# Kernel tuning notes

Hardware: AMD Instinct MI355X
Metric: run time of the kernel (lower is better)

The kernel has to match this reference:

```python
import jax, jax.numpy as jnp
import numpy as np

EMBED_DIM = 1024
NUM_HEADS = 8
HEAD_DIM = EMBED_DIM // NUM_HEADS
SCALING = HEAD_DIM ** -0.5
SEQ_LEN = 2048
BATCH = 4


def setup_inputs() -> dict:
    key = jax.random.key(0)
    ks = jax.random.split(key, 12)
    s = 0.02
    d = EMBED_DIM
    return {
        "q": jax.random.normal(ks[0], (SEQ_LEN, BATCH, d), jnp.float32),
        "k": jax.random.normal(ks[1], (SEQ_LEN, BATCH, d), jnp.float32),
        "v": jax.random.normal(ks[2], (SEQ_LEN, BATCH, d), jnp.float32),
        # Linear weights stored as (in, out): y = x @ W + b
        "Wq": jax.random.normal(ks[3], (d, d), jnp.float32) * s,
        "bq": jnp.zeros((d,), jnp.float32),
        "Wk": jax.random.normal(ks[4], (d, d), jnp.float32) * s,
        "bk": jnp.zeros((d,), jnp.float32),
        "Wv": jax.random.normal(ks[5], (d, d), jnp.float32) * s,
        "bv": jnp.zeros((d,), jnp.float32),
        "Wo": jax.random.normal(ks[6], (d, d), jnp.float32) * s,
        "bo": jnp.zeros((d,), jnp.float32),
    }


def _to_head(x):
    # 'l n (h e) -> n h l e'
    l, n, _ = x.shape
    return x.reshape(l, n, NUM_HEADS, HEAD_DIM).transpose(1, 2, 0, 3)


def reference(q, k, v, Wq, bq, Wk, bk, Wv, bv, Wo, bo):
    l = q.shape[0]  # src_len
    m = k.shape[0]  # tgt_len
    qp = (q @ Wq + bq) * SCALING          # (l, n, d)
    kp = k @ Wk + bk                       # (m, n, d)
    vp = v @ Wv + bv                       # (m, n, d) -- V shared across heads
    qh = _to_head(qp)                      # (n, h, l, e)
    kh = _to_head(kp)                      # (n, h, m, e)
    scores = jnp.einsum('nhle,nhme->nhlm', qh, kh)  # (n, h, l, m)
    mask = jnp.triu(jnp.ones((l, m), bool), k=1)    # True above diagonal
    scores = jnp.where(mask[None, None], -jnp.inf, scores)
    w = jax.nn.softmax(scores, axis=-1)    # (n, h, l, m)
    w_mean = w.mean(axis=1)                # head-averaged weights (n, l, m)
    attn = jnp.einsum('nlm,mne->lne', w_mean, vp)   # (l, n, d)
    out = attn @ Wo + bo                   # (l, n, d)
    return out, w_mean
```

## Files before the change

### kernel.cpp

```cpp
#include <hip/hip_runtime.h>


#define L_SEQ 2048
#define NBATCH 4
#define DMODEL 1024
#define NHEAD 8
#define SCALING 0.08838834764831845f
#define NQ (2048L * 4 * 1024)

typedef _Float16 f16x8 __attribute__((ext_vector_type(8)));
typedef float f32x4 __attribute__((ext_vector_type(4)));

#define GLOBAL_AS __attribute__((address_space(1)))
#define LDS_AS __attribute__((address_space(3)))

__device__ __forceinline__ unsigned short f2h_bits(float x) {
  _Float16 h = (_Float16)x;
  return __builtin_bit_cast(unsigned short, h);
}

__device__ __forceinline__ void gl_lds16(const void* g, void* l) {
  __builtin_amdgcn_global_load_lds((GLOBAL_AS void*)g, (LDS_AS void*)l, 16, 0, 0);
}

__global__ __launch_bounds__(256) void zero1(float4* __restrict__ a, long n4)
{
  float4 z = {0.f, 0.f, 0.f, 0.f};
  long stride = (long)gridDim.x * 256;
  for (long i = (long)blockIdx.x * 256 + threadIdx.x; i < n4; i += stride)
    a[i] = z;
}

__global__ __launch_bounds__(256) void cvt3(
    const float* __restrict__ q, const float* __restrict__ k,
    const float* __restrict__ v, _Float16* __restrict__ xh)
{
  long i = ((long)blockIdx.x * 256 + threadIdx.x) * 8;
  if (i >= 3 * NQ) return;
  int which = (int)(i / NQ);
  const float* src = which == 0 ? q : (which == 1 ? k : v);
  long off = i - (long)which * NQ;
  float4 a = *(const float4*)(src + off);
  float4 b = *(const float4*)(src + off + 4);
  f16x8 h;
  h[0] = (_Float16)a.x; h[1] = (_Float16)a.y; h[2] = (_Float16)a.z; h[3] = (_Float16)a.w;
  h[4] = (_Float16)b.x; h[5] = (_Float16)b.y; h[6] = (_Float16)b.z; h[7] = (_Float16)b.w;
  *(f16x8*)(xh + i) = h;
}

template <bool AF16, bool BF16>
__global__ __launch_bounds__(256) void gemm16(
    const void* __restrict__ Ap, long lda, long a_bs,
    const void* __restrict__ Bp, long ldb, long b_bs,
    float* __restrict__ C, long ldc, long c_bs,
    _Float16* __restrict__ Ch, long ldch, long ch_bs,
    const float* __restrict__ bias, int bias_row, float alpha, int K,
    int causal, int cmode)
{
  __shared__ __align__(16) _Float16 As[128][64];
  __shared__ __align__(16) _Float16 Bs[128][64];
  const int tid = threadIdx.x;
  const int lane = tid & 63, wv = tid >> 6;
  const int g = lane >> 4, cc = lane & 15;
  const int wm = wv >> 1, wn = wv & 1;
  const long m0 = (long)blockIdx.y * 128;
  const long n0 = (long)blockIdx.x * 128;

  const float* Af = nullptr; const _Float16* Ah = nullptr;
  const float* Bf = nullptr; const _Float16* Bh = nullptr;
  if constexpr (AF16) Ah = (const _Float16*)Ap + (long)blockIdx.z * a_bs;
  else                Af = (const float*)Ap + (long)blockIdx.z * a_bs;
  if constexpr (BF16) Bh = (const _Float16*)Bp + (long)blockIdx.z * b_bs;
  else                Bf = (const float*)Bp + (long)blockIdx.z * b_bs;

  int Keff = K;
  if (causal) { int lim = (int)m0 + 128; if (lim < K) Keff = lim; }
  const int NT = Keff >> 6;

  f32x4 acc[4][4] = {};
  char* AsB = (char*)&As[0][0];
  char* BsB = (char*)&Bs[0][0];

  for (int kt = 0; kt < NT; ++kt) {
    const long k0 = (long)kt << 6;
    __syncthreads();
    if constexpr (AF16) {
#pragma unroll
      for (int i = 0; i < 4; ++i) {
        int r = 32 * wv + 8 * i + (lane >> 3);
        int gc = (lane & 7) ^ (r & 7);
        gl_lds16(Ah + (m0 + r) * lda + k0 + gc * 8, &As[32 * wv + 8 * i][0]);
      }
    } else {
#pragma unroll
      for (int p = 0; p < 8; ++p) {
        int r = p * 16 + (tid >> 4);
        float4 vv = *(const float4*)(Af + (m0 + r) * lda + k0 + (tid & 15) * 4);
        ushort4 hh;
        hh.x = f2h_bits(vv.x); hh.y = f2h_bits(vv.y);
        hh.z = f2h_bits(vv.z); hh.w = f2h_bits(vv.w);
        *(ushort4*)(AsB + r * 128 + (((tid & 15) * 8) ^ ((r & 7) << 4))) = hh;
      }
    }
    if constexpr (BF16) {
#pragma unroll
      for (int i = 0; i < 4; ++i) {
        int r = 32 * wv + 8 * i + (lane >> 3);
        int gc = (lane & 7) ^ (r & 7);
        gl_lds16(Bh + (n0 + r) * ldb + k0 + gc * 8, &Bs[32 * wv + 8 * i][0]);
      }
    } else {
#pragma unroll
      for (int p = 0; p < 8; ++p) {
        int r = p * 16 + (tid >> 4);
        float4 vv = *(const float4*)(Bf + (n0 + r) * ldb + k0 + (tid & 15) * 4);
        ushort4 hh;
        hh.x = f2h_bits(vv.x); hh.y = f2h_bits(vv.y);
        hh.z = f2h_bits(vv.z); hh.w = f2h_bits(vv.w);
        *(ushort4*)(BsB + r * 128 + (((tid & 15) * 8) ^ ((r & 7) << 4))) = hh;
      }
    }
    __syncthreads();
#pragma unroll
    for (int s = 0; s < 2; ++s) {
      f16x8 af[4], bfr[4];
#pragma unroll
      for (int mi = 0; mi < 4; ++mi) {
        int r = wm * 64 + mi * 16 + cc;
        af[mi] = *(const f16x8*)(AsB + r * 128 + ((s * 64 + 16 * g) ^ ((r & 7) << 4)));
      }
#pragma unroll
      for (int ni = 0; ni < 4; ++ni) {
        int r = wn * 64 + ni * 16 + cc;
        bfr[ni] = *(const f16x8*)(BsB + r * 128 + ((s * 64 + 16 * g) ^ ((r & 7) << 4)));
      }
#pragma unroll
      for (int mi = 0; mi < 4; ++mi)
#pragma unroll
        for (int ni = 0; ni < 4; ++ni)
          acc[mi][ni] = __builtin_amdgcn_mfma_f32_16x16x32_f16(af[mi], bfr[ni], acc[mi][ni], 0, 0, 0);
    }
  }

  float* Cp = C ? C + (long)blockIdx.z * c_bs : nullptr;
  _Float16* Chp = Ch ? Ch + (long)blockIdx.z * ch_bs : nullptr;
#pragma unroll
  for (int ni = 0; ni < 4; ++ni) {
    long col = n0 + wn * 64 + ni * 16 + cc;
    float bcol = (bias && !bias_row) ? bias[col] : 0.0f;
#pragma unroll
    for (int mi = 0; mi < 4; ++mi) {
      long row0 = m0 + wm * 64 + mi * 16 + 4 * g;
#pragma unroll
      for (int rg = 0; rg < 4; ++rg) {
        long row = row0 + rg;
        float b = (bias && bias_row) ? bias[row] : bcol;
        float vv = (acc[mi][ni][rg] + b) * alpha;
        if (Cp) Cp[row * ldc + col] = vv;
        if (Chp) {
          if (cmode == 1) {
            long idx = (((row & 3) * NHEAD + (col >> 7)) * (long)L_SEQ + (row >> 2)) * 128 +
                       (col & 127);
            Chp[idx] = (_Float16)vv;
          } else {
            Chp[row * ldch + col] = (_Float16)vv;
          }
        }
      }
    }
  }
}

__global__ __launch_bounds__(256) void projqk(
    const _Float16* __restrict__ xh, const _Float16* __restrict__ WqT,
    const _Float16* __restrict__ WkT, const float* __restrict__ bq,
    const float* __restrict__ bk, _Float16* __restrict__ qph,
    _Float16* __restrict__ kph)
{
  __shared__ __align__(16) _Float16 As[64][64];
  __shared__ __align__(16) _Float16 Bs[128][64];
  const int tid = threadIdx.x, lane = tid & 63, wv = tid >> 6;
  const int g = lane >> 4, cc = lane & 15;
  const int wm = wv >> 1, wn = wv & 1;
  const int sel = (int)blockIdx.y;
  const _Float16* A = xh + (long)sel * NQ;
  const _Float16* B = sel ? WkT : WqT;
  const float* bias = sel ? bk : bq;
  const float alpha = sel ? 1.0f : SCALING;
  _Float16* dst = sel ? kph : qph;
  const int fi = (int)blockIdx.x;
  const long m0 = (long)(fi >> 3) * 64;
  const long n0 = (long)(fi & 7) * 128;

  f32x4 acc[2][4] = {};
  char* AsB = (char*)&As[0][0];
  char* BsB = (char*)&Bs[0][0];

  for (int kt = 0; kt < 16; ++kt) {
    const long k0 = (long)kt << 6;
    __syncthreads();
#pragma unroll
    for (int i = 0; i < 2; ++i) {
      int r = 16 * wv + 8 * i + (lane >> 3);
      int gc = (lane & 7) ^ (r & 7);
      gl_lds16(A + (m0 + r) * 1024 + k0 + gc * 8, &As[16 * wv + 8 * i][0]);
    }
#pragma unroll
    for (int i = 0; i < 4; ++i) {
      int r = 32 * wv + 8 * i + (lane >> 3);
      int gc = (lane & 7) ^ (r & 7);
      gl_lds16(B + (n0 + r) * 1024 + k0 + gc * 8, &Bs[32 * wv + 8 * i][0]);
    }
    __syncthreads();
#pragma unroll
    for (int s = 0; s < 2; ++s) {
      f16x8 af[2], bfr[4];
#pragma unroll
      for (int mi = 0; mi < 2; ++mi) {
        int r = wm * 32 + mi * 16 + cc;
        af[mi] = *(const f16x8*)(AsB + r * 128 + ((s * 64 + 16 * g) ^ ((r & 7) << 4)));
      }
#pragma unroll
      for (int ni = 0; ni < 4; ++ni) {
        int r = wn * 64 + ni * 16 + cc;
        bfr[ni] = *(const f16x8*)(BsB + r * 128 + ((s * 64 + 16 * g) ^ ((r & 7) << 4)));
      }
#pragma unroll
      for (int mi = 0; mi < 2; ++mi)
#pragma unroll
        for (int ni = 0; ni < 4; ++ni)
          acc[mi][ni] = __builtin_amdgcn_mfma_f32_16x16x32_f16(af[mi], bfr[ni], acc[mi][ni], 0, 0, 0);
    }
  }

#pragma unroll
  for (int ni = 0; ni < 4; ++ni) {
    long col = n0 + wn * 64 + ni * 16 + cc;
    float bcol = bias[col];
#pragma unroll
    for (int mi = 0; mi < 2; ++mi) {
      long row0 = m0 + wm * 32 + mi * 16 + 4 * g;
#pragma unroll
      for (int rg = 0; rg < 4; ++rg) {
        long row = row0 + rg;
        float vv = (acc[mi][ni][rg] + bcol) * alpha;
        long idx = (((row & 3) * NHEAD + (col >> 7)) * (long)L_SEQ + (row >> 2)) * 128 +
                   (col & 127);
        dst[idx] = (_Float16)vv;
      }
    }
  }
}

__global__ __launch_bounds__(256) void proj64(
    const _Float16* __restrict__ Ap, long lda, long a_bs,
    const _Float16* __restrict__ Bp, long ldb, long b_bs,
    _Float16* __restrict__ Ch, long ldch, long ch_bs,
    const float* __restrict__ bias, int bias_row, float alpha, int K,
    int cmode, int ntiles)
{
  __shared__ __align__(16) _Float16 As[64][64];
  __shared__ __align__(16) _Float16 Bs[128][64];
  const int tid = threadIdx.x, lane = tid & 63, wv = tid >> 6;
  const int g = lane >> 4, cc = lane & 15;
  const int wm = wv >> 1, wn = wv & 1;
  const int fi = (int)blockIdx.x;
  const int by = fi / ntiles, nc = fi % ntiles;
  const long m0 = (long)by * 64;
  const long n0 = (long)nc * 128;
  const _Float16* A = Ap + (long)blockIdx.z * a_bs;
  const _Float16* B = Bp + (long)blockIdx.z * b_bs;
  const int NT = K >> 6;

  f32x4 acc[2][4] = {};
  char* AsB = (char*)&As[0][0];
  char* BsB = (char*)&Bs[0][0];

  for (int kt = 0; kt < NT; ++kt) {
    const long k0 = (long)kt << 6;
    __syncthreads();
#pragma unroll
    for (int i = 0; i < 2; ++i) {
      int r = 16 * wv + 8 * i + (lane >> 3);
      int gc = (lane & 7) ^ (r & 7);
      gl_lds16(A + (m0 + r) * lda + k0 + gc * 8, &As[16 * wv + 8 * i][0]);
    }
#pragma unroll
    for (int i = 0; i < 4; ++i) {
      int r = 32 * wv + 8 * i + (lane >> 3);
      int gc = (lane & 7) ^ (r & 7);
      gl_lds16(B + (n0 + r) * ldb + k0 + gc * 8, &Bs[32 * wv + 8 * i][0]);
    }
    __syncthreads();
#pragma unroll
    for (int s = 0; s < 2; ++s) {
      f16x8 af[2], bfr[4];
#pragma unroll
      for (int mi = 0; mi < 2; ++mi) {
        int r = wm * 32 + mi * 16 + cc;
        af[mi] = *(const f16x8*)(AsB + r * 128 + ((s * 64 + 16 * g) ^ ((r & 7) << 4)));
      }
#pragma unroll
      for (int ni = 0; ni < 4; ++ni) {
        int r = wn * 64 + ni * 16 + cc;
        bfr[ni] = *(const f16x8*)(BsB + r * 128 + ((s * 64 + 16 * g) ^ ((r & 7) << 4)));
      }
#pragma unroll
      for (int mi = 0; mi < 2; ++mi)
#pragma unroll
        for (int ni = 0; ni < 4; ++ni)
          acc[mi][ni] = __builtin_amdgcn_mfma_f32_16x16x32_f16(af[mi], bfr[ni], acc[mi][ni], 0, 0, 0);
    }
  }

  _Float16* Chp = Ch + (long)blockIdx.z * ch_bs;
#pragma unroll
  for (int ni = 0; ni < 4; ++ni) {
    long col = n0 + wn * 64 + ni * 16 + cc;
    float bcol = bias_row ? 0.0f : bias[col];
#pragma unroll
    for (int mi = 0; mi < 2; ++mi) {
      long row0 = m0 + wm * 32 + mi * 16 + 4 * g;
#pragma unroll
      for (int rg = 0; rg < 4; ++rg) {
        long row = row0 + rg;
        float b = bias_row ? bias[row] : bcol;
        float vv = (acc[mi][ni][rg] + b) * alpha;
        if (cmode == 1) {
          long idx = (((row & 3) * NHEAD + (col >> 7)) * (long)L_SEQ + (row >> 2)) * 128 +
                     (col & 127);
          Chp[idx] = (_Float16)vv;
        } else {
          Chp[row * ldch + col] = (_Float16)vv;
        }
      }
    }
  }
}

__global__ __launch_bounds__(256) void out_gemm16(
    const _Float16* __restrict__ wm16, const _Float16* __restrict__ voT,
    const float* __restrict__ bo, float* __restrict__ out)
{
  __shared__ __align__(16) _Float16 As[64][64];
  __shared__ __align__(16) _Float16 Bs[128][64];
  const int tid = threadIdx.x, lane = tid & 63, wv = tid >> 6;
  const int g = lane >> 4, cc = lane & 15;
  const int wm = wv >> 1, wn = wv & 1;
  const int fi = (int)blockIdx.x;
  const int by = 31 - (fi >> 5);
  const int j = fi & 31;
  const int nb = j >> 3, nc = j & 7;
  const long m0 = (long)by * 64;
  const long n0 = (long)nc * 128;
  const _Float16* A = wm16 + (long)nb * L_SEQ * L_SEQ;
  const _Float16* B = voT + (long)nb * 2048L * 1024;
  const int NT = by + 1;

  f32x4 acc[2][4] = {};
  char* AsB = (char*)&As[0][0];
  char* BsB = (char*)&Bs[0][0];

  for (int kt = 0; kt < NT; ++kt) {
    const long k0 = (long)kt << 6;
    __syncthreads();
#pragma unroll
    for (int i = 0; i < 2; ++i) {
      int r = 16 * wv + 8 * i + (lane >> 3);
      int gc = (lane & 7) ^ (r & 7);
      gl_lds16(A + (m0 + r) * 2048 + k0 + gc * 8, &As[16 * wv + 8 * i][0]);
    }
#pragma unroll
    for (int i = 0; i < 4; ++i) {
      int r = 32 * wv + 8 * i + (lane >> 3);
      int gc = (lane & 7) ^ (r & 7);
      gl_lds16(B + (n0 + r) * 2048 + k0 + gc * 8, &Bs[32 * wv + 8 * i][0]);
    }
    __syncthreads();
#pragma unroll
    for (int s = 0; s < 2; ++s) {
      f16x8 af[2], bfr[4];
#pragma unroll
      for (int mi = 0; mi < 2; ++mi) {
        int r = wm * 32 + mi * 16 + cc;
        af[mi] = *(const f16x8*)(AsB + r * 128 + ((s * 64 + 16 * g) ^ ((r & 7) << 4)));
      }
#pragma unroll
      for (int ni = 0; ni < 4; ++ni) {
        int r = wn * 64 + ni * 16 + cc;
        bfr[ni] = *(const f16x8*)(BsB + r * 128 + ((s * 64 + 16 * g) ^ ((r & 7) << 4)));
      }
#pragma unroll
      for (int mi = 0; mi < 2; ++mi)
#pragma unroll
        for (int ni = 0; ni < 4; ++ni)
          acc[mi][ni] = __builtin_amdgcn_mfma_f32_16x16x32_f16(af[mi], bfr[ni], acc[mi][ni], 0, 0, 0);
    }
  }

#pragma unroll
  for (int ni = 0; ni < 4; ++ni) {
    long col = n0 + wn * 64 + ni * 16 + cc;
    float b = bo[col];
#pragma unroll
    for (int mi = 0; mi < 2; ++mi) {
      long l0 = m0 + wm * 32 + mi * 16 + 4 * g;
#pragma unroll
      for (int rg = 0; rg < 4; ++rg)
        out[(l0 + rg) * 4096 + nb * 1024 + col] = acc[mi][ni][rg] + b;
    }
  }
}

__global__ __launch_bounds__(256) void transpose3(
    const float* __restrict__ s0, const float* __restrict__ s1,
    const float* __restrict__ s2,
    _Float16* __restrict__ d0, _Float16* __restrict__ d1,
    _Float16* __restrict__ d2)
{
  __shared__ _Float16 tile[32][33];
  const float* in = blockIdx.z == 0 ? s0 : (blockIdx.z == 1 ? s1 : s2);
  _Float16* outp = blockIdx.z == 0 ? d0 : (blockIdx.z == 1 ? d1 : d2);
  int r0 = blockIdx.y * 32, c0 = blockIdx.x * 32;
  for (int i = threadIdx.y; i < 32; i += 8)
    tile[i][threadIdx.x] = (_Float16)in[(long)(r0 + i) * 1024 + c0 + threadIdx.x];
  __syncthreads();
  for (int i = threadIdx.y; i < 32; i += 8)
    outp[(long)(c0 + i) * 1024 + r0 + threadIdx.x] = tile[threadIdx.x][i];
}

__global__ __launch_bounds__(256) void bias_proj(
    const float* __restrict__ bv, const float* __restrict__ Wo, float* __restrict__ bvo)
{
  int j = blockIdx.x * 256 + threadIdx.x;
  float acc = 0.f;
  for (int i = 0; i < DMODEL; ++i) acc += bv[i] * Wo[(long)i * DMODEL + j];
  bvo[j] = acc;
}

__global__ __launch_bounds__(256) void s1_kernel(
    const _Float16* __restrict__ qph, const _Float16* __restrict__ kph,
    float* __restrict__ Zsum)
{
  __shared__ __align__(16) _Float16 Qs[64][128];
  __shared__ __align__(16) _Float16 Ks[64][128];
  const int tid = threadIdx.x, lane = tid & 63, w = tid >> 6;
  const int g = lane >> 4, cc = lane & 15;
  const int h = blockIdx.y, nb = blockIdx.z;
  int fi = 79 - (int)blockIdx.x;
  int by, seg;
  if (fi < 8)       { by = fi;                  seg = 0; }
  else if (fi < 24) { int t = fi - 8;  by = 8  + (t >> 1); seg = t & 1; }
  else if (fi < 48) { int t = fi - 24; by = 16 + t / 3;    seg = t % 3; }
  else              { int t = fi - 48; by = 24 + (t >> 2); seg = t & 3; }
  const int lb = by * 64;
  const int c0 = seg * 8;
  const int cEnd = min(c0 + 8, by + 1);
  const int srow = lane >> 4, scl = lane & 15;
  const long hb = ((long)(nb * NHEAD + h)) * L_SEQ * 128;
  char* QsB = (char*)&Qs[0][0];
  char* KsB = (char*)&Ks[0][0];

#pragma unroll
  for (int i = 0; i < 4; ++i) {
    int r = 16 * w + 4 * i + srow;
    int gc = scl ^ (r & 7);
    gl_lds16(&qph[hb + (long)(lb + r) * 128 + gc * 8], &Qs[16 * w + 4 * i][0]);
  }
  auto stageK = [&](int ch) {
#pragma unroll
    for (int i = 0; i < 4; ++i) {
      int r = 16 * w + 4 * i + srow;
      int gc = scl ^ (r & 7);
      gl_lds16(&kph[hb + (long)(ch * 64 + r) * 128 + gc * 8], &Ks[16 * w + 4 * i][0]);
    }
  };
  stageK(c0);
  __syncthreads();

  f16x8 qf[4];
  {
    int r = 16 * w + cc;
#pragma unroll
    for (int s = 0; s < 4; ++s)
      qf[s] = *(const f16x8*)(QsB + r * 256 + ((64 * s + 16 * g) ^ ((r & 7) << 4)));
  }

  f32x4 zacc = {0.f, 0.f, 0.f, 0.f};
  const int l0 = lb + 16 * w + 4 * g;
  for (int ch = c0; ch < cEnd; ++ch) {
#pragma unroll
    for (int t = 0; t < 4; ++t) {
      int kr = 16 * t + cc;
      f32x4 acc = {0.f, 0.f, 0.f, 0.f};
#pragma unroll
      for (int s = 0; s < 4; ++s) {
        f16x8 kf = *(const f16x8*)(KsB + kr * 256 + ((64 * s + 16 * g) ^ ((kr & 7) << 4)));
        acc = __builtin_amdgcn_mfma_f32_16x16x32_f16(qf[s], kf, acc, 0, 0, 0);
      }
      int m = ch * 64 + 16 * t + cc;
#pragma unroll
      for (int rg = 0; rg < 4; ++rg) {
        float e = __expf(acc[rg]);
        zacc[rg] += (m <= l0 + rg) ? e : 0.f;
      }
    }
    if (ch + 1 < cEnd) {
      __syncthreads();
      stageK(ch + 1);
      __syncthreads();
    }
  }
#pragma unroll
  for (int rg = 0; rg < 4; ++rg) {
    float vv = zacc[rg];
    vv += __shfl_xor(vv, 1, 16);
    vv += __shfl_xor(vv, 2, 16);
    vv += __shfl_xor(vv, 4, 16);
    vv += __shfl_xor(vv, 8, 16);
    if (cc == 0)
      atomicAdd(&Zsum[((long)nb * NHEAD + h) * L_SEQ + l0 + rg], vv);
  }
}

__global__ __launch_bounds__(256) void zero_fill(float* __restrict__ wmean)
{
  int t = (int)blockIdx.x, nb = (int)blockIdx.y;
  int by = 0, rem = t;
  while (rem >= 15 - by) { rem -= 15 - by; ++by; }
  const int mc = by + 1 + rem;
  const int tr = threadIdx.x >> 1, th = threadIdx.x & 1;
  float4 z4 = {0.f, 0.f, 0.f, 0.f};
  float* p = wmean + (long)nb * L_SEQ * L_SEQ + (long)(by * 128 + tr) * L_SEQ +
             mc * 128 + th * 64;
#pragma unroll
  for (int j = 0; j < 16; ++j) ((float4*)p)[j] = z4;
}

__global__ __launch_bounds__(256) void s2_kernel(
    const _Float16* __restrict__ qph, const _Float16* __restrict__ kph,
    const float* __restrict__ Zsum, float* __restrict__ wmean,
    _Float16* __restrict__ wm16)
{
  __shared__ __align__(16) _Float16 Qs[64][128];
  __shared__ __align__(16) _Float16 Ks[64][128];
  __shared__ float zl[NHEAD][64];
  const int tid = threadIdx.x, lane = tid & 63, w = tid >> 6;
  const int g = lane >> 4, cc = lane & 15;
  const int nb = blockIdx.y;
  int b = (int)blockIdx.x;
  int bx = (b & 7) * 66 + (b >> 3);
  int by = 0, rem = bx;
  while (rem > by) { rem -= by + 1; ++by; }
  const int mc = rem;
  const int lb = by * 64, mb = mc * 64;
  const bool diag = (mc == by);
  const int srow = lane >> 4, scl = lane & 15;
  char* QsB = (char*)&Qs[0][0];
  char* KsB = (char*)&Ks[0][0];

  for (int i = tid; i < NHEAD * 64; i += 256)
    zl[i >> 6][i & 63] =
        1.0f / (8.0f * Zsum[((long)nb * NHEAD + (i >> 6)) * L_SEQ + lb + (i & 63)]);

  auto stage = [&](int h) {
    const long qb = ((long)(nb * NHEAD + h) * L_SEQ + lb) * 128;
    const long kb = ((long)(nb * NHEAD + h) * L_SEQ + mb) * 128;
#pragma unroll
    for (int i = 0; i < 4; ++i) {
      int r = 16 * w + 4 * i + srow;
      int gc = scl ^ (r & 7);
      gl_lds16(&qph[qb + (long)r * 128 + gc * 8], &Qs[16 * w + 4 * i][0]);
      gl_lds16(&kph[kb + (long)r * 128 + gc * 8], &Ks[16 * w + 4 * i][0]);
    }
  };
  stage(0);
  __syncthreads();

  f32x4 wacc[4] = {};
  const int l0 = lb + 16 * w + 4 * g;
  for (int h = 0; h < NHEAD; ++h) {
    f16x8 qf[4];
    int qr = 16 * w + cc;
#pragma unroll
    for (int s = 0; s < 4; ++s)
      qf[s] = *(const f16x8*)(QsB + qr * 256 + ((64 * s + 16 * g) ^ ((qr & 7) << 4)));
    f32x4 zv = *(const f32x4*)&zl[h][16 * w + 4 * g];
#pragma unroll
    for (int t = 0; t < 4; ++t) {
      int kr = 16 * t + cc;
      f32x4 acc = {0.f, 0.f, 0.f, 0.f};
#pragma unroll
      for (int s = 0; s < 4; ++s) {
        f16x8 kf = *(const f16x8*)(KsB + kr * 256 + ((64 * s + 16 * g) ^ ((kr & 7) << 4)));
        acc = __builtin_amdgcn_mfma_f32_16x16x32_f16(qf[s], kf, acc, 0, 0, 0);
      }
      int m = mb + 16 * t + cc;
#pragma unroll
      for (int rg = 0; rg < 4; ++rg) {
        float e = __expf(acc[rg]) * zv[rg];
        wacc[t][rg] += (!diag || m <= l0 + rg) ? e : 0.f;
      }
    }
    if (h + 1 < NHEAD) {
      __syncthreads();
      stage(h + 1);
      __syncthreads();
    }
  }
  float* wout = wmean + (long)nb * L_SEQ * L_SEQ;
  _Float16* w16 = wm16 + (long)nb * L_SEQ * L_SEQ;
#pragma unroll
  for (int t = 0; t < 4; ++t) {
    int m = mb + 16 * t + cc;
#pragma unroll
    for (int rg = 0; rg < 4; ++rg) {
      long idx = (long)(l0 + rg) * L_SEQ + m;
      wout[idx] = wacc[t][rg];
      w16[idx] = (_Float16)wacc[t][rg];
    }
  }
}

extern "C" void kernel_launch(void* const* d_in, const int* in_sizes, int n_in,
                              void* d_out, int out_size, void* d_ws, size_t ws_size,
                              hipStream_t stream)
{
  const float* q  = (const float*)d_in[0];
  const float* k  = (const float*)d_in[1];
  const float* v  = (const float*)d_in[2];
  const float* Wq = (const float*)d_in[3];
  const float* bq = (const float*)d_in[4];
  const float* Wk = (const float*)d_in[5];
  const float* bk = (const float*)d_in[6];
  const float* Wv = (const float*)d_in[7];
  const float* bv = (const float*)d_in[8];
  const float* Wo = (const float*)d_in[9];
  const float* bo = (const float*)d_in[10];

  float* out = (float*)d_out;
  float* wmean = out + (long)L_SEQ * NBATCH * DMODEL;

  if (ws_size < (140UL << 20)) return;

  char* ws = (char*)d_ws;
  _Float16* xh   = (_Float16*)(ws);
  _Float16* qph  = (_Float16*)(ws + (48L << 20));
  _Float16* kph  = (_Float16*)(ws + (64L << 20));
  _Float16* voT  = (_Float16*)(ws + (80L << 20));
  _Float16* wm16 = (_Float16*)(ws + (96L << 20));
  _Float16* WqT  = (_Float16*)(ws + (130L << 20));
  _Float16* WkT  = (_Float16*)(ws + (132L << 20));
  _Float16* WoT  = (_Float16*)(ws + (134L << 20));
  _Float16* WvoT = (_Float16*)(ws + (136L << 20));
  float*    bvo  = (float*)   (ws + (138L << 20));
  float*    Zsum = (float*)   (ws + (138L << 20) + (1L << 16));

  zero1<<<dim3(64, 1, 1), 256, 0, stream>>>(
      (float4*)Zsum, (long)NBATCH * NHEAD * L_SEQ / 4);
  transpose3<<<dim3(32, 32, 3), dim3(32, 8, 1), 0, stream>>>(
      Wq, Wk, Wo, WqT, WkT, WoT);
  bias_proj<<<dim3(4, 1, 1), 256, 0, stream>>>(bv, Wo, bvo);
  gemm16<true, false><<<dim3(8, 8, 1), 256, 0, stream>>>(
      WoT, 1024, 0, Wv, 1024, 0,
      (float*)nullptr, 0, 0, WvoT, 1024, 0,
      (const float*)nullptr, 0, 1.0f, 1024, 0, 0);
  cvt3<<<dim3(12288, 1, 1), 256, 0, stream>>>(q, k, v, xh);
  projqk<<<dim3(1024, 2, 1), 256, 0, stream>>>(xh, WqT, WkT, bq, bk, qph, kph);
  proj64<<<dim3(256, 1, 4), 256, 0, stream>>>(
      WvoT, 1024, 0, xh + 2 * NQ, 4096, 1024, voT, 2048, 2048L * 1024,
      bvo, 1, 1.0f, 1024, 0, 16);
  s1_kernel<<<dim3(80, NHEAD, NBATCH), 256, 0, stream>>>(qph, kph, Zsum);
  zero_fill<<<dim3(120, 4, 1), 256, 0, stream>>>(wmean);
  s2_kernel<<<dim3(528, NBATCH, 1), 256, 0, stream>>>(qph, kph, Zsum, wmean, wm16);
  out_gemm16<<<dim3(1024, 1, 1), 256, 0, stream>>>(wm16, voT, bo, out);
}
```

Before: 325.6 us.

## Widen s2 key tile to 128 columns and merge prep kernels into one launch

Measured after the change: 314.5 us. -3.4%, faster.

```diff
diff --git a/kernel.cpp b/kernel.cpp
--- a/kernel.cpp
+++ b/kernel.cpp
@@ -23,12 +23,38 @@
   __builtin_amdgcn_global_load_lds((GLOBAL_AS void*)g, (LDS_AS void*)l, 16, 0, 0);
 }
 
-__global__ __launch_bounds__(256) void zero1(float4* __restrict__ a, long n4)
-{
-  float4 z = {0.f, 0.f, 0.f, 0.f};
-  long stride = (long)gridDim.x * 256;
-  for (long i = (long)blockIdx.x * 256 + threadIdx.x; i < n4; i += stride)
-    a[i] = z;
+__global__ __launch_bounds__(256) void prep(
+    const float* __restrict__ Wq, const float* __restrict__ Wk,
+    const float* __restrict__ Wo,
+    _Float16* __restrict__ WqT, _Float16* __restrict__ WkT,
+    _Float16* __restrict__ WoT,
+    const float* __restrict__ bv, float* __restrict__ bvo,
+    float4* __restrict__ Zsum4)
+{
+  const int z = (int)blockIdx.z;
+  const int tid = threadIdx.y * 32 + threadIdx.x;
+  if (z == 3) {
+    if (blockIdx.y == 0 && blockIdx.x < 4) {
+      int j = blockIdx.x * 256 + tid;
+      float acc = 0.f;
+      for (int i = 0; i < DMODEL; ++i) acc += bv[i] * Wo[(long)i * DMODEL + j];
+      bvo[j] = acc;
+    } else if (blockIdx.y == 1 || blockIdx.y == 2) {
+      long idx = ((long)(blockIdx.y - 1) * 32 + blockIdx.x) * 256 + tid;
+      if (idx < (long)NBATCH * NHEAD * L_SEQ / 4)
+        Zsum4[idx] = (float4){0.f, 0.f, 0.f, 0.f};
+    }
+    return;
+  }
+  __shared__ _Float16 tile[32][33];
+  const float* in = z == 0 ? Wq : (z == 1 ? Wk : Wo);
+  _Float16* outp = z == 0 ? WqT : (z == 1 ? WkT : WoT);
+  int r0 = blockIdx.y * 32, c0 = blockIdx.x * 32;
+  for (int i = threadIdx.y; i < 32; i += 8)
+    tile[i][threadIdx.x] = (_Float16)in[(long)(r0 + i) * 1024 + c0 + threadIdx.x];
+  __syncthreads();
+  for (int i = threadIdx.y; i < 32; i += 8)
+    outp[(long)(c0 + i) * 1024 + r0 + threadIdx.x] = tile[threadIdx.x][i];
 }
 
 __global__ __launch_bounds__(256) void cvt3(
@@ -410,32 +436,6 @@
         out[(l0 + rg) * 4096 + nb * 1024 + col] = acc[mi][ni][rg] + b;
     }
   }
-}
-
-__global__ __launch_bounds__(256) void transpose3(
-    const float* __restrict__ s0, const float* __restrict__ s1,
-    const float* __restrict__ s2,
-    _Float16* __restrict__ d0, _Float16* __restrict__ d1,
-    _Float16* __restrict__ d2)
-{
-  __shared__ _Float16 tile[32][33];
-  const float* in = blockIdx.z == 0 ? s0 : (blockIdx.z == 1 ? s1 : s2);
-  _Float16* outp = blockIdx.z == 0 ? d0 : (blockIdx.z == 1 ? d1 : d2);
-  int r0 = blockIdx.y * 32, c0 = blockIdx.x * 32;
-  for (int i = threadIdx.y; i < 32; i += 8)
-    tile[i][threadIdx.x] = (_Float16)in[(long)(r0 + i) * 1024 + c0 + threadIdx.x];
-  __syncthreads();
-  for (int i = threadIdx.y; i < 32; i += 8)
-    outp[(long)(c0 + i) * 1024 + r0 + threadIdx.x] = tile[threadIdx.x][i];
-}
-
-__global__ __launch_bounds__(256) void bias_proj(
-    const float* __restrict__ bv, const float* __restrict__ Wo, float* __restrict__ bvo)
-{
-  int j = blockIdx.x * 256 + threadIdx.x;
-  float acc = 0.f;
-  for (int i = 0; i < DMODEL; ++i) acc += bv[i] * Wo[(long)i * DMODEL + j];
-  bvo[j] = acc;
 }
 
 __global__ __launch_bounds__(256) void s1_kernel(
@@ -543,18 +543,19 @@
     _Float16* __restrict__ wm16)
 {
   __shared__ __align__(16) _Float16 Qs[64][128];
-  __shared__ __align__(16) _Float16 Ks[64][128];
+  __shared__ __align__(16) _Float16 Ks[128][128];
   __shared__ float zl[NHEAD][64];
   const int tid = threadIdx.x, lane = tid & 63, w = tid >> 6;
   const int g = lane >> 4, cc = lane & 15;
   const int nb = blockIdx.y;
   int b = (int)blockIdx.x;
-  int bx = (b & 7) * 66 + (b >> 3);
-  int by = 0, rem = bx;
-  while (rem > by) { rem -= by + 1; ++by; }
+  int bx = (b & 7) * 34 + (b >> 3);
+  int rem = 271 - bx;
+  int by = 0;
+  while (rem >= (by >> 1) + 1) { rem -= (by >> 1) + 1; ++by; }
   const int mc = rem;
-  const int lb = by * 64, mb = mc * 64;
-  const bool diag = (mc == by);
+  const int lb = by * 64, mb = mc * 128;
+  const bool diag = (mb + 127 > lb);
   const int srow = lane >> 4, scl = lane & 15;
   char* QsB = (char*)&Qs[0][0];
   char* KsB = (char*)&Ks[0][0];
@@ -571,13 +572,18 @@
       int r = 16 * w + 4 * i + srow;
       int gc = scl ^ (r & 7);
       gl_lds16(&qph[qb + (long)r * 128 + gc * 8], &Qs[16 * w + 4 * i][0]);
-      gl_lds16(&kph[kb + (long)r * 128 + gc * 8], &Ks[16 * w + 4 * i][0]);
+    }
+#pragma unroll
+    for (int i = 0; i < 8; ++i) {
+      int r = 32 * w + 4 * i + srow;
+      int gc = scl ^ (r & 7);
+      gl_lds16(&kph[kb + (long)r * 128 + gc * 8], &Ks[32 * w + 4 * i][0]);
     }
   };
   stage(0);
   __syncthreads();
 
-  f32x4 wacc[4] = {};
+  f32x4 wacc[8] = {};
   const int l0 = lb + 16 * w + 4 * g;
   for (int h = 0; h < NHEAD; ++h) {
     f16x8 qf[4];
@@ -587,7 +593,7 @@
       qf[s] = *(const f16x8*)(QsB + qr * 256 + ((64 * s + 16 * g) ^ ((qr & 7) << 4)));
     f32x4 zv = *(const f32x4*)&zl[h][16 * w + 4 * g];
 #pragma unroll
-    for (int t = 0; t < 4; ++t) {
+    for (int t = 0; t < 8; ++t) {
       int kr = 16 * t + cc;
       f32x4 acc = {0.f, 0.f, 0.f, 0.f};
 #pragma unroll
@@ -611,7 +617,7 @@
   float* wout = wmean + (long)nb * L_SEQ * L_SEQ;
   _Float16* w16 = wm16 + (long)nb * L_SEQ * L_SEQ;
 #pragma unroll
-  for (int t = 0; t < 4; ++t) {
+  for (int t = 0; t < 8; ++t) {
     int m = mb + 16 * t + cc;
 #pragma unroll
     for (int rg = 0; rg < 4; ++rg) {
@@ -656,11 +662,8 @@
   float*    bvo  = (float*)   (ws + (138L << 20));
   float*    Zsum = (float*)   (ws + (138L << 20) + (1L << 16));
 
-  zero1<<<dim3(64, 1, 1), 256, 0, stream>>>(
-      (float4*)Zsum, (long)NBATCH * NHEAD * L_SEQ / 4);
-  transpose3<<<dim3(32, 32, 3), dim3(32, 8, 1), 0, stream>>>(
-      Wq, Wk, Wo, WqT, WkT, WoT);
-  bias_proj<<<dim3(4, 1, 1), 256, 0, stream>>>(bv, Wo, bvo);
+  prep<<<dim3(32, 32, 4), dim3(32, 8, 1), 0, stream>>>(
+      Wq, Wk, Wo, WqT, WkT, WoT, bv, bvo, (float4*)Zsum);
   gemm16<true, false><<<dim3(8, 8, 1), 256, 0, stream>>>(
       WoT, 1024, 0, Wv, 1024, 0,
       (float*)nullptr, 0, 0, WvoT, 1024, 0,
@@ -672,6 +675,6 @@
       bvo, 1, 1.0f, 1024, 0, 16);
   s1_kernel<<<dim3(80, NHEAD, NBATCH), 256, 0, stream>>>(qph, kph, Zsum);
   zero_fill<<<dim3(120, 4, 1), 256, 0, stream>>>(wmean);
-  s2_kernel<<<dim3(528, NBATCH, 1), 256, 0, stream>>>(qph, kph, Zsum, wmean, wm16);
+  s2_kernel<<<dim3(272, NBATCH, 1), 256, 0, stream>>>(qph, kph, Zsum, wmean, wm16);
   out_gemm16<<<dim3(1024, 1, 1), 256, 0, stream>>>(wm16, voT, bo, out);
 }
```
